# Optimization experiments

Hardware: AMD Instinct MI355X
Metric: run time of the kernel (lower is better)

The kernel has to match this reference:

```python
import jax, jax.numpy as jnp
import numpy as np

B, S, E, H, D = 2, 2048, 512, 8, 64
NEG = -1e10


def setup_inputs() -> dict:
    key = jax.random.key(0)
    k1, k2, k3, k4, k5, k6 = jax.random.split(key, 6)
    inputs = jax.random.normal(k1, (B, S, E), dtype=jnp.float32)
    keys = jax.random.normal(k2, (B, S, H, D), dtype=jnp.float32)
    values = jax.random.normal(k3, (B, S, H, D), dtype=jnp.float32)
    # xavier-uniform style scale for square weights
    lim = float(np.sqrt(6.0 / (E + H * D)))
    query_weights = jax.random.uniform(k4, (E, H * D), minval=-lim, maxval=lim, dtype=jnp.float32)
    output_weights = jax.random.uniform(k5, (H * D, E), minval=-lim, maxval=lim, dtype=jnp.float32)
    mask = jax.random.randint(k6, (B, S, S), 0, 2).astype(jnp.bool_)
    return {"inputs": inputs, "keys": keys, "values": values,
            "query_weights": query_weights, "output_weights": output_weights,
            "mask": mask}


def reference(inputs, keys, values, query_weights, output_weights, mask):
    # project queries: (B,S,E) @ (E,H*D) -> (B,S,H,D)
    q = jnp.matmul(inputs, query_weights).reshape(B, S, H, D)
    # scores: (B,H,Sq,Sk)
    scores = jnp.einsum('bqhd,bkhd->bhqk', q, keys) / jnp.sqrt(jnp.float32(D))
    # masked_fill(mask, -1e10); mask broadcasts over heads
    scores = jnp.where(mask[:, None, :, :], jnp.float32(NEG), scores)
    probs = jax.nn.softmax(scores, axis=-1)
    # (B,H,Sq,Sk) x (B,Sk,H,D) -> (B,Sq,H,D)
    out = jnp.einsum('bhqk,bkhd->bqhd', probs, values)
    out = out.reshape(B, S, H * D)
    return jnp.matmul(out, output_weights)
```

## Files before the change

kernel.cpp:

```cpp
#include <hip/hip_runtime.h>
#include <hip/hip_bf16.h>

namespace {

constexpr int B = 2, S = 2048, E = 512, H = 8, D = 64, HD = 512;
constexpr float SL = 0.125f * 1.44269504f;
constexpr int PLD = 40;

typedef __attribute__((ext_vector_type(8))) short bf16x8;
typedef __attribute__((ext_vector_type(4))) unsigned short u16x4;
typedef __attribute__((ext_vector_type(4))) float f32x4;
typedef __attribute__((ext_vector_type(4))) float float4v;

__device__ __forceinline__ ushort f2b(float x) {
  __hip_bfloat16 h = __float2bfloat16(x);
  return *reinterpret_cast<const ushort*>(&h);
}

__global__ __launch_bounds__(256) void prep_fused_kernel(
    const float* __restrict__ K, const float* __restrict__ V,
    const float* __restrict__ Wq, const float* __restrict__ Wo,
    const int* __restrict__ maskp,
    ushort* __restrict__ Kbf, ushort* __restrict__ Vtbf,
    ushort* __restrict__ Wtq, ushort* __restrict__ Wto,
    uint4* __restrict__ keep4) {
  const int bid = blockIdx.x;
  const int t = threadIdx.x;
  if (bid < 512) {
    __shared__ __align__(16) ushort Vn[64][76];
    const int kt = bid & 31;
    const int bh = bid >> 5;
    const int b = bh >> 3, h = bh & 7;
    const int k0 = kt * 64;
#pragma unroll
    for (int i = 0; i < 4; ++i) {
      int c = i * 256 + t;
      int kk = c >> 4, d4 = (c & 15) * 4;
      size_t g = ((size_t)(b * 2048 + k0 + kk) * 8 + h) * 64 + d4;
      float4v kv = *(const float4v*)(K + g);
      float4v vv = *(const float4v*)(V + g);
      u16x4 kp = {f2b(kv.x), f2b(kv.y), f2b(kv.z), f2b(kv.w)};
      u16x4 vp = {f2b(vv.x), f2b(vv.y), f2b(vv.z), f2b(vv.w)};
      *(u16x4*)(Kbf + ((size_t)(bh * 2048 + k0 + kk)) * 64 + d4) = kp;
      *(u16x4*)&Vn[kk][d4] = vp;
    }
    __syncthreads();
#pragma unroll
    for (int i = 0; i < 2; ++i) {
      int c = i * 256 + t;
      int kc8 = (c & 7) * 8, d = c >> 3;
      union { ushort u[8]; bf16x8 v; } p;
#pragma unroll
      for (int j = 0; j < 8; ++j) p.u[j] = Vn[kc8 + j][d];
      *(bf16x8*)(Vtbf + ((size_t)(bh * 64 + d)) * 2048 + k0 + kc8) = p.v;
    }
  } else if (bid < 640) {
    __shared__ __align__(16) ushort T[64][68];
    const int idx = bid - 512;
    const float* Wsrc = (idx >> 6) ? Wo : Wq;
    ushort* Wdst = (idx >> 6) ? Wto : Wtq;
    const int x = idx & 63;
    const int k0 = (x & 7) * 64, n0 = (x >> 3) * 64;
#pragma unroll
    for (int i = 0; i < 4; ++i) {
      int c = i * 256 + t;
      int kk = c >> 4, n4 = (c & 15) * 4;
      float4v v = *(const float4v*)(Wsrc + (size_t)(k0 + kk) * 512 + n0 + n4);
      u16x4 p = {f2b(v.x), f2b(v.y), f2b(v.z), f2b(v.w)};
      *(u16x4*)&T[kk][n4] = p;
    }
    __syncthreads();
#pragma unroll
    for (int i = 0; i < 2; ++i) {
      int c = i * 256 + t;
      int n = c >> 3, k8 = (c & 7) * 8;
      union { ushort u[8]; bf16x8 v; } p;
#pragma unroll
      for (int j = 0; j < 8; ++j) p.u[j] = T[k8 + j][n];
      *(bf16x8*)(Wdst + (size_t)(n0 + n) * 512 + k0 + k8) = p.v;
    }
  } else {
    const int wid = (bid - 640) * 4 + (t >> 6);
    const int row = wid >> 3, c = wid & 7;
    const int lane = t & 63;
    const int4 v = *((const int4*)(maskp + (size_t)row * 2048 + c * 256) + lane);
    unsigned long long bx = __ballot(v.x == 0);
    unsigned long long by = __ballot(v.y == 0);
    unsigned long long bz = __ballot(v.z == 0);
    unsigned long long bw = __ballot(v.w == 0);
    if (lane == 0)
      keep4[(size_t)row * 16 + c * 2] = uint4{(uint)bx, (uint)by, (uint)bz, (uint)bw};
    if (lane == 32)
      keep4[(size_t)row * 16 + c * 2 + 1] =
          uint4{(uint)(bx >> 32), (uint)(by >> 32), (uint)(bz >> 32), (uint)(bw >> 32)};
  }
}

__global__ __launch_bounds__(256) void proj_out_kernel(
    const ushort* __restrict__ A, const ushort* __restrict__ Wt, float* __restrict__ C) {
  __shared__ __align__(16) ushort As[64][PLD];
  __shared__ __align__(16) ushort Ws[64][PLD];

  const int tid = threadIdx.x;
  const int lane = tid & 63;
  const int w = tid >> 6;
  const int col = lane & 15;
  const int quad = lane >> 4;
  const int m0 = blockIdx.y * 64;
  const int n0 = blockIdx.x * 64;
  const int wm = (w & 1) * 32;
  const int wn = (w >> 1) * 32;
  const int ar = tid >> 2;
  const int ak = (tid & 3) * 8;
  const int wn2 = tid >> 2;
  const int wkc = (tid & 3) * 8;

  f32x4 acc[2][2];
#pragma unroll
  for (int i = 0; i < 2; ++i)
#pragma unroll
    for (int j = 0; j < 2; ++j) acc[i][j] = f32x4{0.f, 0.f, 0.f, 0.f};

  const ushort* Ap = A + (size_t)(m0 + ar) * 512 + ak;
  const ushort* Wp = Wt + (size_t)(n0 + wn2) * 512 + wkc;
  bf16x8 apre = *(const bf16x8*)Ap;
  bf16x8 wp = *(const bf16x8*)Wp;

  for (int kt = 0; kt < 16; ++kt) {
    if (kt) __syncthreads();
    *(bf16x8*)&As[ar][ak] = apre;
    *(bf16x8*)&Ws[wn2][wkc] = wp;
    if (kt < 15) {
      const int k1 = (kt + 1) * 32;
      apre = *(const bf16x8*)(Ap + k1);
      wp = *(const bf16x8*)(Wp + k1);
    }
    __syncthreads();

    bf16x8 ah[2], wb[2];
#pragma unroll
    for (int i = 0; i < 2; ++i)
      ah[i] = *(const bf16x8*)&As[wm + i * 16 + col][quad * 8];
#pragma unroll
    for (int j = 0; j < 2; ++j)
      wb[j] = *(const bf16x8*)&Ws[wn + j * 16 + col][quad * 8];
#pragma unroll
    for (int i = 0; i < 2; ++i)
#pragma unroll
      for (int j = 0; j < 2; ++j)
        acc[i][j] = __builtin_amdgcn_mfma_f32_16x16x32_bf16(ah[i], wb[j], acc[i][j], 0, 0, 0);
  }

#pragma unroll
  for (int i = 0; i < 2; ++i)
#pragma unroll
    for (int j = 0; j < 2; ++j)
#pragma unroll
      for (int r = 0; r < 4; ++r)
        C[(size_t)(m0 + wm + i * 16 + (quad << 2) + r) * 512 + n0 + wn + j * 16 + col] =
            acc[i][j][r];
}

__global__ __launch_bounds__(256, 2) void flash_attn_kernel(
    const float* __restrict__ inp, const ushort* __restrict__ Wtq,
    const ushort* __restrict__ Kbf, const ushort* __restrict__ Vtbf,
    const uint4* __restrict__ keep4, ushort* __restrict__ Op) {
  __shared__ __align__(16) union SM {
    ushort PQ[64][72];
    struct { float red[3][64][68]; float lred[3][64]; } r;
  } sm;

  const int bid0 = blockIdx.x;
  const int bid = (bid0 & 7) * 64 + (bid0 >> 3);
  const int qt = bid & 31;
  const int bh = bid >> 5;
  const int b = bh >> 3, h = bh & 7;
  const int q0 = qt * 64;
  const int tid = threadIdx.x, lane = tid & 63, w = tid >> 6;
  const int col = lane & 15, quad = lane >> 4, quad4 = quad * 4;
  const int wm = (w & 1) * 32;
  const int wn = (w >> 1) * 32;

  {
    const int ar = tid >> 2;
    const int ak = (tid & 3) * 8;

    f32x4 qacc[2][2];
#pragma unroll
    for (int i = 0; i < 2; ++i)
#pragma unroll
      for (int j = 0; j < 2; ++j) qacc[i][j] = f32x4{0.f, 0.f, 0.f, 0.f};

    const float* Ap = inp + (size_t)(b * 2048 + q0 + ar) * 512 + ak;
    const ushort* Wp = Wtq + (size_t)(h * 64 + ar) * 512 + ak;
    float4v a0p = *(const float4v*)Ap;
    float4v a1p = *(const float4v*)(Ap + 4);
    bf16x8 wp = *(const bf16x8*)Wp;

    for (int kt = 0; kt < 16; ++kt) {
      if (kt) __syncthreads();
      {
        union { ushort u[8]; bf16x8 v; } ap;
        ap.u[0] = f2b(a0p.x); ap.u[1] = f2b(a0p.y); ap.u[2] = f2b(a0p.z); ap.u[3] = f2b(a0p.w);
        ap.u[4] = f2b(a1p.x); ap.u[5] = f2b(a1p.y); ap.u[6] = f2b(a1p.z); ap.u[7] = f2b(a1p.w);
        *(bf16x8*)&sm.PQ[ar][ak] = ap.v;
        *(bf16x8*)&sm.PQ[ar][40 + ak] = wp;
      }
      if (kt < 15) {
        const int k1 = (kt + 1) * 32;
        a0p = *(const float4v*)(Ap + k1);
        a1p = *(const float4v*)(Ap + k1 + 4);
        wp = *(const bf16x8*)(Wp + k1);
      }
      __syncthreads();

      bf16x8 ah[2], wb[2];
#pragma unroll
      for (int i = 0; i < 2; ++i)
        ah[i] = *(const bf16x8*)&sm.PQ[wm + i * 16 + col][quad * 8];
#pragma unroll
      for (int j = 0; j < 2; ++j)
        wb[j] = *(const bf16x8*)&sm.PQ[wn + j * 16 + col][40 + quad * 8];
#pragma unroll
      for (int i = 0; i < 2; ++i)
#pragma unroll
        for (int j = 0; j < 2; ++j)
          qacc[i][j] = __builtin_amdgcn_mfma_f32_16x16x32_bf16(ah[i], wb[j], qacc[i][j], 0, 0, 0);
    }

    __syncthreads();
#pragma unroll
    for (int i = 0; i < 2; ++i)
#pragma unroll
      for (int j = 0; j < 2; ++j)
#pragma unroll
        for (int r = 0; r < 4; ++r)
          sm.PQ[wm + i * 16 + quad4 + r][wn + j * 16 + col] = f2b(qacc[i][j][r] * SL);
    __syncthreads();
  }

  bf16x8 qb[4][2];
#pragma unroll
  for (int j = 0; j < 4; ++j)
#pragma unroll
    for (int hf = 0; hf < 2; ++hf)
      qb[j][hf] = *(const bf16x8*)&sm.PQ[j * 16 + col][hf * 32 + quad * 8];

  f32x4 oacc[4][4];
#pragma unroll
  for (int j = 0; j < 4; ++j)
#pragma unroll
    for (int c = 0; c < 4; ++c) oacc[j][c] = f32x4{0.f, 0.f, 0.f, 0.f};
  f32x4 lacc[4];
#pragma unroll
  for (int j = 0; j < 4; ++j) lacc[j] = f32x4{0.f, 0.f, 0.f, 0.f};

  union { ushort u[8]; bf16x8 v; } onesu;
#pragma unroll
  for (int j = 0; j < 8; ++j) onesu.u[j] = 0x3F80;
  const bf16x8 onesB = onesu.v;

  const uint4* kr0 = keep4 + (size_t)(b * 2048 + q0 + col) * 16;
  const ushort* Kp = Kbf + (size_t)bh * 131072 + (size_t)(w * 32 + col) * 64 + quad * 8;
  const ushort* Vp = Vtbf + (size_t)bh * 131072 + (size_t)col * 2048 + w * 32 + quad * 8;
  const int mshift = 8 * w + quad;

  auto LOADK = [&](bf16x8 (&d)[2][2], const int kt) {
#pragma unroll
    for (int t = 0; t < 2; ++t)
#pragma unroll
      for (int hf = 0; hf < 2; ++hf)
        d[t][hf] = *(const bf16x8*)(Kp + kt * 8192 + t * 1024 + hf * 32);
  };
  auto LOADM = [&](uint4 (&d)[4], const int kt) {
#pragma unroll
    for (int j = 0; j < 4; ++j) d[j] = kr0[j * 256 + kt];
  };
  auto COMPUTE = [&](const bf16x8 (&ka)[2][2], const uint4 (&kwj)[4], const int kt) {
    bf16x8 vv[4];
#pragma unroll
    for (int j = 0; j < 4; ++j) {
      f32x4 sc0 = f32x4{0.f, 0.f, 0.f, 0.f};
      f32x4 sc1 = f32x4{0.f, 0.f, 0.f, 0.f};
      sc0 = __builtin_amdgcn_mfma_f32_16x16x32_bf16(ka[0][0], qb[j][0], sc0, 0, 0, 0);
      sc0 = __builtin_amdgcn_mfma_f32_16x16x32_bf16(ka[0][1], qb[j][1], sc0, 0, 0, 0);
      sc1 = __builtin_amdgcn_mfma_f32_16x16x32_bf16(ka[1][0], qb[j][0], sc1, 0, 0, 0);
      sc1 = __builtin_amdgcn_mfma_f32_16x16x32_bf16(ka[1][1], qb[j][1], sc1, 0, 0, 0);
      if (j == 0) {
#pragma unroll
        for (int c = 0; c < 4; ++c)
          vv[c] = *(const bf16x8*)(Vp + kt * 128 + c * 32768);
      }
      const uint mx_ = kwj[j].x >> mshift, my_ = kwj[j].y >> mshift,
                 mz_ = kwj[j].z >> mshift, mw_ = kwj[j].w >> mshift;
      uint Xa0, Xa1, Xb0, Xb1;
      {
        float p0 = (mx_ & 1u) ? exp2f(sc0[0]) : 0.f;
        float p1 = (my_ & 1u) ? exp2f(sc0[1]) : 0.f;
        float p2 = (mz_ & 1u) ? exp2f(sc0[2]) : 0.f;
        float p3 = (mw_ & 1u) ? exp2f(sc0[3]) : 0.f;
        __hip_bfloat162 lo = __float22bfloat162_rn(float2{p0, p1});
        __hip_bfloat162 hi = __float22bfloat162_rn(float2{p2, p3});
        Xa0 = *reinterpret_cast<uint*>(&lo);
        Xa1 = *reinterpret_cast<uint*>(&hi);
      }
      {
        float p0 = ((mx_ >> 4) & 1u) ? exp2f(sc1[0]) : 0.f;
        float p1 = ((my_ >> 4) & 1u) ? exp2f(sc1[1]) : 0.f;
        float p2 = ((mz_ >> 4) & 1u) ? exp2f(sc1[2]) : 0.f;
        float p3 = ((mw_ >> 4) & 1u) ? exp2f(sc1[3]) : 0.f;
        __hip_bfloat162 lo = __float22bfloat162_rn(float2{p0, p1});
        __hip_bfloat162 hi = __float22bfloat162_rn(float2{p2, p3});
        Xb0 = *reinterpret_cast<uint*>(&lo);
        Xb1 = *reinterpret_cast<uint*>(&hi);
      }
      auto a32 = __builtin_amdgcn_permlane32_swap(Xa0, Xb0, false, false);
      auto a16 = __builtin_amdgcn_permlane16_swap(a32[0], a32[1], false, false);
      auto b32 = __builtin_amdgcn_permlane32_swap(Xa1, Xb1, false, false);
      auto b16 = __builtin_amdgcn_permlane16_swap(b32[0], b32[1], false, false);
      union { uint u[4]; bf16x8 v; } pu;
      pu.u[0] = a16[0]; pu.u[1] = b16[0]; pu.u[2] = a16[1]; pu.u[3] = b16[1];
      const bf16x8 pa = pu.v;
      lacc[j] = __builtin_amdgcn_mfma_f32_16x16x32_bf16(pa, onesB, lacc[j], 0, 0, 0);
#pragma unroll
      for (int c = 0; c < 4; ++c)
        oacc[j][c] = __builtin_amdgcn_mfma_f32_16x16x32_bf16(pa, vv[c], oacc[j][c], 0, 0, 0);
    }
  };

  bf16x8 kA[2][2], kB[2][2];
  uint4 kwA[4], kwB[4];
  LOADK(kA, 0);
#pragma unroll 1
  for (int kt = 0; kt < 16; kt += 2) {
    LOADM(kwA, kt);
    LOADK(kB, kt + 1);
    COMPUTE(kA, kwA, kt);
    LOADM(kwB, kt + 1);
    if (kt < 14) LOADK(kA, kt + 2);
    COMPUTE(kB, kwB, kt + 1);
  }

  __syncthreads();
  if (w > 0) {
    const int wi = w - 1;
#pragma unroll
    for (int j = 0; j < 4; ++j)
#pragma unroll
      for (int c = 0; c < 4; ++c)
        *(f32x4*)&sm.r.red[wi][c * 16 + col][j * 16 + quad4] = oacc[j][c];
    if (col == 0)
#pragma unroll
      for (int j = 0; j < 4; ++j)
        *(f32x4*)&sm.r.lred[wi][j * 16 + quad4] = lacc[j];
  }
  __syncthreads();
  if (w == 0) {
#pragma unroll
    for (int j = 0; j < 4; ++j) {
#pragma unroll
      for (int c = 0; c < 4; ++c) {
        f32x4 s = oacc[j][c];
#pragma unroll
        for (int i = 0; i < 3; ++i)
          s += *(const f32x4*)&sm.r.red[i][c * 16 + col][j * 16 + quad4];
        oacc[j][c] = s;
      }
      f32x4 ls = lacc[j];
#pragma unroll
      for (int i = 0; i < 3; ++i)
        ls += *(const f32x4*)&sm.r.lred[i][j * 16 + quad4];
      lacc[j] = ls;
    }
#pragma unroll
    for (int j = 0; j < 4; ++j) {
#pragma unroll
      for (int c = 0; c < 4; ++c)
        *(f32x4*)&sm.r.red[0][c * 16 + col][j * 16 + quad4] = oacc[j][c];
      if (col == 0) *(f32x4*)&sm.r.lred[0][j * 16 + quad4] = lacc[j];
    }
  }
  __syncthreads();

  {
    const int q = tid >> 2, d0 = (tid & 3) * 16;
    const float inv = 1.f / sm.r.lred[0][q];
    union { ushort u[16]; bf16x8 v[2]; } ob;
#pragma unroll
    for (int dd = 0; dd < 16; ++dd)
      ob.u[dd] = f2b(sm.r.red[0][d0 + dd][q] * inv);
    ushort* dst = Op + (size_t)(b * S + q0 + q) * HD + h * D + d0;
    *(bf16x8*)dst = ob.v[0];
    *(bf16x8*)(dst + 8) = ob.v[1];
  }
}

}

extern "C" void kernel_launch(void* const* d_in, const int* in_sizes, int n_in,
                              void* d_out, int out_size, void* d_ws, size_t ws_size,
                              hipStream_t stream) {
  const float* inputs = (const float*)d_in[0];
  const float* keys   = (const float*)d_in[1];
  const float* values = (const float*)d_in[2];
  const float* wq     = (const float*)d_in[3];
  const float* wo     = (const float*)d_in[4];
  const int*   maskp  = (const int*)d_in[5];
  float* out = (float*)d_out;

  ushort* Kbf  = (ushort*)d_out;
  ushort* Vtbf = Kbf + (size_t)2097152;

  char* ws = (char*)d_ws;
  ushort* attnb = (ushort*)ws;
  uint4*  keep4 = (uint4*)(ws + (4 << 20));
  ushort* Wtq   = (ushort*)(ws + (5 << 20));
  ushort* Wto   = (ushort*)(ws + (5 << 20) + (512 << 10));

  prep_fused_kernel<<<dim3(8832), dim3(256), 0, stream>>>(keys, values, wq, wo, maskp,
                                                          Kbf, Vtbf, Wtq, Wto, keep4);
  flash_attn_kernel<<<dim3(512), dim3(256), 0, stream>>>(inputs, Wtq, Kbf, Vtbf, keep4, attnb);
  proj_out_kernel<<<dim3(8, 64), dim3(256), 0, stream>>>(attnb, Wto, out);
}
```

Baseline: 168.4 us.

## Stage K/V tiles through double-buffered LDS with register prefetch in flash attention

Replaces the per-wave direct global loads of K and V with cooperative block-wide loads into register prefetch buffers, which are then written into double-buffered shared-memory tiles. Each wave then reads its MFMA fragments from LDS. The aim is coalesced global access and overlap of the next tile's load with the current tile's compute. It also batches the score MFMAs and wraps the MFMA groups in s_setprio, and it drops the XCD-aware block index swizzle. The cost is larger LDS use (about 54KB per block, which may limit occupancy to 2 blocks), two barriers per tile pair, and extra registers for the prefetch buffers.

After: 209.1 us. 1.24x slower.

```diff
diff --git a/kernel.cpp b/kernel.cpp
--- a/kernel.cpp
+++ b/kernel.cpp
@@ -166,12 +166,12 @@
     const ushort* __restrict__ Kbf, const ushort* __restrict__ Vtbf,
     const uint4* __restrict__ keep4, ushort* __restrict__ Op) {
   __shared__ __align__(16) union SM {
+    struct { ushort Ks[2][128][72]; ushort Vt[2][64][136]; } m;
     ushort PQ[64][72];
     struct { float red[3][64][68]; float lred[3][64]; } r;
   } sm;
 
-  const int bid0 = blockIdx.x;
-  const int bid = (bid0 & 7) * 64 + (bid0 >> 3);
+  const int bid = blockIdx.x;
   const int qt = bid & 31;
   const int bh = bid >> 5;
   const int b = bh >> 3, h = bh & 7;
@@ -245,6 +245,7 @@
 #pragma unroll
     for (int hf = 0; hf < 2; ++hf)
       qb[j][hf] = *(const bf16x8*)&sm.PQ[j * 16 + col][hf * 32 + quad * 8];
+  __syncthreads();
 
   f32x4 oacc[4][4];
 #pragma unroll
@@ -261,87 +262,126 @@
   const bf16x8 onesB = onesu.v;
 
   const uint4* kr0 = keep4 + (size_t)(b * 2048 + q0 + col) * 16;
-  const ushort* Kp = Kbf + (size_t)bh * 131072 + (size_t)(w * 32 + col) * 64 + quad * 8;
-  const ushort* Vp = Vtbf + (size_t)bh * 131072 + (size_t)col * 2048 + w * 32 + quad * 8;
+  const ushort* Kbase = Kbf + (size_t)bh * 131072;
+  const ushort* Vbase = Vtbf + (size_t)bh * 131072;
   const int mshift = 8 * w + quad;
 
-  auto LOADK = [&](bf16x8 (&d)[2][2], const int kt) {
-#pragma unroll
-    for (int t = 0; t < 2; ++t)
-#pragma unroll
-      for (int hf = 0; hf < 2; ++hf)
-        d[t][hf] = *(const bf16x8*)(Kp + kt * 8192 + t * 1024 + hf * 32);
-  };
-  auto LOADM = [&](uint4 (&d)[4], const int kt) {
-#pragma unroll
-    for (int j = 0; j < 4; ++j) d[j] = kr0[j * 256 + kt];
-  };
-  auto COMPUTE = [&](const bf16x8 (&ka)[2][2], const uint4 (&kwj)[4], const int kt) {
-    bf16x8 vv[4];
-#pragma unroll
-    for (int j = 0; j < 4; ++j) {
-      f32x4 sc0 = f32x4{0.f, 0.f, 0.f, 0.f};
-      f32x4 sc1 = f32x4{0.f, 0.f, 0.f, 0.f};
-      sc0 = __builtin_amdgcn_mfma_f32_16x16x32_bf16(ka[0][0], qb[j][0], sc0, 0, 0, 0);
-      sc0 = __builtin_amdgcn_mfma_f32_16x16x32_bf16(ka[0][1], qb[j][1], sc0, 0, 0, 0);
-      sc1 = __builtin_amdgcn_mfma_f32_16x16x32_bf16(ka[1][0], qb[j][0], sc1, 0, 0, 0);
-      sc1 = __builtin_amdgcn_mfma_f32_16x16x32_bf16(ka[1][1], qb[j][1], sc1, 0, 0, 0);
-      if (j == 0) {
-#pragma unroll
-        for (int c = 0; c < 4; ++c)
-          vv[c] = *(const bf16x8*)(Vp + kt * 128 + c * 32768);
-      }
-      const uint mx_ = kwj[j].x >> mshift, my_ = kwj[j].y >> mshift,
-                 mz_ = kwj[j].z >> mshift, mw_ = kwj[j].w >> mshift;
-      uint Xa0, Xa1, Xb0, Xb1;
-      {
-        float p0 = (mx_ & 1u) ? exp2f(sc0[0]) : 0.f;
-        float p1 = (my_ & 1u) ? exp2f(sc0[1]) : 0.f;
-        float p2 = (mz_ & 1u) ? exp2f(sc0[2]) : 0.f;
-        float p3 = (mw_ & 1u) ? exp2f(sc0[3]) : 0.f;
-        __hip_bfloat162 lo = __float22bfloat162_rn(float2{p0, p1});
-        __hip_bfloat162 hi = __float22bfloat162_rn(float2{p2, p3});
-        Xa0 = *reinterpret_cast<uint*>(&lo);
-        Xa1 = *reinterpret_cast<uint*>(&hi);
-      }
-      {
-        float p0 = ((mx_ >> 4) & 1u) ? exp2f(sc1[0]) : 0.f;
-        float p1 = ((my_ >> 4) & 1u) ? exp2f(sc1[1]) : 0.f;
-        float p2 = ((mz_ >> 4) & 1u) ? exp2f(sc1[2]) : 0.f;
-        float p3 = ((mw_ >> 4) & 1u) ? exp2f(sc1[3]) : 0.f;
-        __hip_bfloat162 lo = __float22bfloat162_rn(float2{p0, p1});
-        __hip_bfloat162 hi = __float22bfloat162_rn(float2{p2, p3});
-        Xb0 = *reinterpret_cast<uint*>(&lo);
-        Xb1 = *reinterpret_cast<uint*>(&hi);
-      }
-      auto a32 = __builtin_amdgcn_permlane32_swap(Xa0, Xb0, false, false);
-      auto a16 = __builtin_amdgcn_permlane16_swap(a32[0], a32[1], false, false);
-      auto b32 = __builtin_amdgcn_permlane32_swap(Xa1, Xb1, false, false);
-      auto b16 = __builtin_amdgcn_permlane16_swap(b32[0], b32[1], false, false);
-      union { uint u[4]; bf16x8 v; } pu;
-      pu.u[0] = a16[0]; pu.u[1] = b16[0]; pu.u[2] = a16[1]; pu.u[3] = b16[1];
-      const bf16x8 pa = pu.v;
-      lacc[j] = __builtin_amdgcn_mfma_f32_16x16x32_bf16(pa, onesB, lacc[j], 0, 0, 0);
-#pragma unroll
-      for (int c = 0; c < 4; ++c)
-        oacc[j][c] = __builtin_amdgcn_mfma_f32_16x16x32_bf16(pa, vv[c], oacc[j][c], 0, 0, 0);
-    }
-  };
-
-  bf16x8 kA[2][2], kB[2][2];
-  uint4 kwA[4], kwB[4];
-  LOADK(kA, 0);
+#define LOADG(KP, VP, T)                                                   \
+  do {                                                                     \
+    const int k1_ = (T) * 128;                                             \
+    _Pragma("unroll") for (int i_ = 0; i_ < 4; ++i_) {                     \
+      int c_ = i_ * 256 + tid;                                             \
+      KP[i_] = *(const bf16x8*)(Kbase + (size_t)k1_ * 64 + c_ * 8);        \
+      int d_ = c_ >> 4, k8_ = (c_ & 15) * 8;                               \
+      VP[i_] = *(const bf16x8*)(Vbase + (size_t)d_ * 2048 + k1_ + k8_);    \
+    }                                                                      \
+  } while (0)
+
+#define STAGE(BUF, KP, VP)                                                 \
+  do {                                                                     \
+    _Pragma("unroll") for (int i_ = 0; i_ < 4; ++i_) {                     \
+      int c_ = i_ * 256 + tid;                                             \
+      *(bf16x8*)&sm.m.Ks[BUF][c_ >> 3][(c_ & 7) * 8] = KP[i_];             \
+      int d_ = c_ >> 4, k8_ = (c_ & 15) * 8;                               \
+      *(bf16x8*)&sm.m.Vt[BUF][d_][k8_] = VP[i_];                           \
+    }                                                                      \
+  } while (0)
+
+#define LOADM(MW, T)                                                       \
+  do {                                                                     \
+    _Pragma("unroll") for (int j_ = 0; j_ < 4; ++j_) MW[j_] = kr0[j_ * 256 + (T)]; \
+  } while (0)
+
+#define COMPUTE(BUF, MW)                                                          \
+  do {                                                                            \
+    bf16x8 ka_[2][2];                                                             \
+    _Pragma("unroll") for (int t_ = 0; t_ < 2; ++t_)                              \
+      _Pragma("unroll") for (int hf_ = 0; hf_ < 2; ++hf_)                         \
+        ka_[t_][hf_] =                                                            \
+            *(const bf16x8*)&sm.m.Ks[BUF][w * 32 + t_ * 16 + col][hf_ * 32 + quad * 8]; \
+    f32x4 sc_[2][4];                                                              \
+    _Pragma("unroll") for (int t_ = 0; t_ < 2; ++t_)                              \
+      _Pragma("unroll") for (int j_ = 0; j_ < 4; ++j_)                            \
+        sc_[t_][j_] = f32x4{0.f, 0.f, 0.f, 0.f};                                  \
+    __builtin_amdgcn_s_setprio(1);                                                \
+    _Pragma("unroll") for (int t_ = 0; t_ < 2; ++t_)                              \
+      _Pragma("unroll") for (int hf_ = 0; hf_ < 2; ++hf_)                         \
+        _Pragma("unroll") for (int j_ = 0; j_ < 4; ++j_)                          \
+          sc_[t_][j_] = __builtin_amdgcn_mfma_f32_16x16x32_bf16(                  \
+              ka_[t_][hf_], qb[j_][hf_], sc_[t_][j_], 0, 0, 0);                   \
+    __builtin_amdgcn_s_setprio(0);                                                \
+    bf16x8 vb_[4];                                                                \
+    _Pragma("unroll") for (int c_ = 0; c_ < 4; ++c_)                              \
+      vb_[c_] = *(const bf16x8*)&sm.m.Vt[BUF][c_ * 16 + col][w * 32 + quad * 8];  \
+    _Pragma("unroll") for (int j_ = 0; j_ < 4; ++j_) {                            \
+      const uint mx_ = MW[j_].x >> mshift, my_ = MW[j_].y >> mshift,              \
+                 mz_ = MW[j_].z >> mshift, mw_ = MW[j_].w >> mshift;              \
+      uint Xa0, Xa1, Xb0, Xb1;                                                    \
+      {                                                                           \
+        float p0 = (mx_ & 1u) ? exp2f(sc_[0][j_][0]) : 0.f;                       \
+        float p1 = (my_ & 1u) ? exp2f(sc_[0][j_][1]) : 0.f;                       \
+        float p2 = (mz_ & 1u) ? exp2f(sc_[0][j_][2]) : 0.f;                       \
+        float p3 = (mw_ & 1u) ? exp2f(sc_[0][j_][3]) : 0.f;                       \
+        __hip_bfloat162 lo = __float22bfloat162_rn(float2{p0, p1});               \
+        __hip_bfloat162 hi = __float22bfloat162_rn(float2{p2, p3});               \
+        Xa0 = *reinterpret_cast<uint*>(&lo);                                      \
+        Xa1 = *reinterpret_cast<uint*>(&hi);                                      \
+      }                                                                           \
+      {                                                                           \
+        float p0 = ((mx_ >> 4) & 1u) ? exp2f(sc_[1][j_][0]) : 0.f;                \
+        float p1 = ((my_ >> 4) & 1u) ? exp2f(sc_[1][j_][1]) : 0.f;                \
+        float p2 = ((mz_ >> 4) & 1u) ? exp2f(sc_[1][j_][2]) : 0.f;                \
+        float p3 = ((mw_ >> 4) & 1u) ? exp2f(sc_[1][j_][3]) : 0.f;                \
+        __hip_bfloat162 lo = __float22bfloat162_rn(float2{p0, p1});               \
+        __hip_bfloat162 hi = __float22bfloat162_rn(float2{p2, p3});               \
+        Xb0 = *reinterpret_cast<uint*>(&lo);                                      \
+        Xb1 = *reinterpret_cast<uint*>(&hi);                                      \
+      }                                                                           \
+      auto a32 = __builtin_amdgcn_permlane32_swap(Xa0, Xb0, false, false);        \
+      auto a16 = __builtin_amdgcn_permlane16_swap(a32[0], a32[1], false, false);  \
+      auto b32 = __builtin_amdgcn_permlane32_swap(Xa1, Xb1, false, false);        \
+      auto b16 = __builtin_amdgcn_permlane16_swap(b32[0], b32[1], false, false);  \
+      union { uint u[4]; bf16x8 v; } pu;                                          \
+      pu.u[0] = a16[0]; pu.u[1] = b16[0]; pu.u[2] = a16[1]; pu.u[3] = b16[1];     \
+      const bf16x8 pa = pu.v;                                                     \
+      __builtin_amdgcn_s_setprio(1);                                              \
+      lacc[j_] = __builtin_amdgcn_mfma_f32_16x16x32_bf16(pa, onesB, lacc[j_], 0, 0, 0); \
+      _Pragma("unroll") for (int c_ = 0; c_ < 4; ++c_)                            \
+        oacc[j_][c_] =                                                            \
+            __builtin_amdgcn_mfma_f32_16x16x32_bf16(pa, vb_[c_], oacc[j_][c_], 0, 0, 0); \
+      __builtin_amdgcn_s_setprio(0);                                              \
+    }                                                                             \
+  } while (0)
+
+  bf16x8 kpA[4], vpA[4], kpB[4], vpB[4];
+  uint4 mA[4], mB[4];
+  LOADG(kpA, vpA, 0);
+  LOADM(mA, 0);
+  STAGE(0, kpA, vpA);
+  LOADG(kpB, vpB, 1);
+  LOADM(mB, 1);
+  __syncthreads();
+
 #pragma unroll 1
   for (int kt = 0; kt < 16; kt += 2) {
-    LOADM(kwA, kt);
-    LOADK(kB, kt + 1);
-    COMPUTE(kA, kwA, kt);
-    LOADM(kwB, kt + 1);
-    if (kt < 14) LOADK(kA, kt + 2);
-    COMPUTE(kB, kwB, kt + 1);
-  }
-
-  __syncthreads();
+    if (kt < 14) LOADG(kpA, vpA, kt + 2);
+    STAGE(1, kpB, vpB);
+    COMPUTE(0, mA);
+    if (kt < 14) LOADM(mA, kt + 2);
+    __syncthreads();
+    if (kt < 14) {
+      LOADG(kpB, vpB, kt + 3);
+      STAGE(0, kpA, vpA);
+    }
+    COMPUTE(1, mB);
+    if (kt < 14) LOADM(mB, kt + 3);
+    __syncthreads();
+  }
+#undef LOADG
+#undef STAGE
+#undef LOADM
+#undef COMPUTE
+
   if (w > 0) {
     const int wi = w - 1;
 #pragma unroll
```
